# Performance work log

Measured on AMD Instinct MI355X. Metric: run time of the kernel, lower is better.

The kernel has to match this reference:

```python
import jax, jax.numpy as jnp
import numpy as np

N_NODES = 100000
N_EDGES = 640000
DIM = 128
N_LAYERS = 3

def setup_inputs() -> dict:
    key = jax.random.key(0)
    k1, k2, k3 = jax.random.split(key, 3)
    x = jax.random.normal(k1, (1, N_NODES, DIM), dtype=jnp.float32)
    edge_index = jax.random.randint(k2, (2, N_EDGES), 0, N_NODES, dtype=jnp.int64)
    Ws = jax.random.normal(k3, (N_LAYERS, DIM, DIM), dtype=jnp.float32) * (1.0 / np.sqrt(DIM))
    bs = jnp.zeros((N_LAYERS, DIM), dtype=jnp.float32)
    return {"x": x, "edge_index": edge_index, "Ws": Ws, "bs": bs}

def reference(x, edge_index, Ws, bs):
    # Stacked PyG-style GCNConv layers with ReLU, as in GraphEncoder (gnn_type='gcn').
    # GCNConv: add self-loops, symmetric norm D^-1/2 A D^-1/2, h W, scatter-sum, + bias.
    h = x[0]                                  # [N, D] (squeeze batch dim of 1)
    N = h.shape[0]
    loops = jnp.arange(N, dtype=edge_index.dtype)
    src = jnp.concatenate([edge_index[0], loops])   # [E+N] message sources
    dst = jnp.concatenate([edge_index[1], loops])   # [E+N] aggregation targets
    deg = jax.ops.segment_sum(jnp.ones_like(dst, dtype=h.dtype), dst, num_segments=N)
    dinv = jnp.where(deg > 0, jax.lax.rsqrt(deg), 0.0)
    norm = (dinv[src] * dinv[dst])[:, None]         # [E+N, 1] edge weights
    for l in range(Ws.shape[0]):
        m = norm * (h @ Ws[l])[src]                 # gather + per-edge message
        h = jax.ops.segment_sum(m, dst, num_segments=N) + bs[l]
        h = jax.nn.relu(h)
    return h[None]                                  # [1, N, D]
```

## Files before the change

### kernel.cpp

```cpp
#include <hip/hip_runtime.h>

#define DIM 128
#define MROW 272

typedef unsigned int uint32;
typedef short bf16x8 __attribute__((ext_vector_type(8)));
typedef float f32x4 __attribute__((ext_vector_type(4)));

__device__ __forceinline__ unsigned short f2b(float f) {
    return (unsigned short)((__float_as_uint(f) + 0x8000u) >> 16);
}
__device__ __forceinline__ uint32 packbf2(float lo, float hi) {
    uint32 a = __float_as_uint(lo);
    uint32 b = __float_as_uint(hi);
    return ((a + 0x8000u) >> 16) | ((b + 0x8000u) & 0xffff0000u);
}
__device__ __forceinline__ float bflo(uint32 u) { return __uint_as_float(u << 16); }
__device__ __forceinline__ float bfhi(uint32 u) { return __uint_as_float(u & 0xffff0000u); }

__global__ __launch_bounds__(256) void k_count(const int* __restrict__ dst,
                                               int* __restrict__ cnt, int E) {
    int e = blockIdx.x * 256 + threadIdx.x;
    if (e < E) atomicAdd(&cnt[dst[e]], 1);
}

__global__ __launch_bounds__(256) void k_scaleg(const float* __restrict__ x,
                                                const float* __restrict__ dinv,
                                                uint32* __restrict__ g, int n) {
    int t = blockIdx.x * 256 + threadIdx.x;
    if (t >= n * 64) return;
    int node = t >> 6;
    float dv = dinv[node];
    float2 v = ((const float2*)x)[t];
    g[t] = packbf2(dv * v.x, dv * v.y);
}

__global__ __launch_bounds__(256) void k_scan1(const int* __restrict__ cnt,
                                               int* __restrict__ incl,
                                               int* __restrict__ bsums,
                                               float* __restrict__ dinv, int n) {
    __shared__ int tmp[256];
    int i = blockIdx.x * 256 + threadIdx.x;
    int t = threadIdx.x;
    int c = (i < n) ? cnt[i] : 0;
    if (i < n) dinv[i] = rsqrtf((float)(c + 1));
    tmp[t] = c;
    __syncthreads();
#pragma unroll
    for (int off = 1; off < 256; off <<= 1) {
        int v = (t >= off) ? tmp[t - off] : 0;
        __syncthreads();
        tmp[t] += v;
        __syncthreads();
    }
    if (i < n) incl[i] = tmp[t];
    if (t == 255) bsums[blockIdx.x] = tmp[255];
}

__global__ __launch_bounds__(512) void k_scan2(int* __restrict__ bsums, int nb) {
    __shared__ int tmp[512];
    int t = threadIdx.x;
    tmp[t] = (t < nb) ? bsums[t] : 0;
    __syncthreads();
#pragma unroll
    for (int off = 1; off < 512; off <<= 1) {
        int v = (t >= off) ? tmp[t - off] : 0;
        __syncthreads();
        tmp[t] += v;
        __syncthreads();
    }
    if (t < nb) bsums[t] = (t == 0) ? 0 : tmp[t - 1];
}

__global__ __launch_bounds__(256) void k_scan3(int* __restrict__ incl,
                                               const int* __restrict__ bsums, int n) {
    int i = blockIdx.x * 256 + threadIdx.x;
    if (i < n) incl[i] += bsums[blockIdx.x];
}

__global__ __launch_bounds__(256) void k_fill(const int* __restrict__ src,
                                              const int* __restrict__ dst,
                                              int* __restrict__ incl,
                                              int* __restrict__ srcs, int E) {
    int e = blockIdx.x * 256 + threadIdx.x;
    if (e >= E) return;
    int p = atomicSub(&incl[dst[e]], 1) - 1;
    srcs[p] = src[e];
}

__global__ __launch_bounds__(256) void k_prepW(const float* __restrict__ Ws,
                                               short* __restrict__ Wb, int total) {
    int t = blockIdx.x * 256 + threadIdx.x;
    if (t >= total) return;
    int layer = t >> 14;
    int idx = t & 16383;
    int j = idx & 7;
    int l = (idx >> 3) & 63;
    int f = idx >> 9;
    int ks = f & 3;
    int cs = (f >> 2) & 1;
    int w = f >> 3;
    int nn = w * 32 + cs * 16 + (l & 15);
    int kk = ks * 32 + (l >> 4) * 8 + j;
    Wb[t] = (short)f2b(Ws[(size_t)layer * DIM * DIM + kk * DIM + nn]);
}

__global__ __launch_bounds__(256) void k_layer(const uint32* __restrict__ g,
                                               const int* __restrict__ srcs,
                                               const int* __restrict__ rowptr,
                                               const float* __restrict__ dinv,
                                               const short* __restrict__ Wb,
                                               const float* __restrict__ bias,
                                               uint32* __restrict__ Gn,
                                               float* __restrict__ Out,
                                               int n, int E, int final_layer) {
    __shared__ __align__(16) char smem[32 * MROW];
    int tid = threadIdx.x;
    int row0 = blockIdx.x * 32;
    int w = tid >> 6;
    int l = tid & 63;
    int lr = l & 15;
    int lg = l >> 4;

    const bf16x8* wb = (const bf16x8*)Wb;
    bf16x8 bfrag[2][4];
#pragma unroll
    for (int cs = 0; cs < 2; ++cs)
#pragma unroll
        for (int ks = 0; ks < 4; ++ks)
            bfrag[cs][ks] = wb[((w * 2 + cs) * 4 + ks) * 64 + l];

    int hw = tid >> 5;
    int sub = tid & 31;
    const uint2* g2 = (const uint2*)g;
#pragma unroll
    for (int i = 0; i < 4; ++i) {
        int nl = hw * 4 + i;
        int node = row0 + nl;
        uint2 o = make_uint2(0u, 0u);
        if (node < n) {
            int start = rowptr[node];
            int end = (node + 1 < n) ? rowptr[node + 1] : E;
            uint2 us = g2[(size_t)node * 32 + sub];
            float a0 = bflo(us.x), a1 = bfhi(us.x), a2 = bflo(us.y), a3 = bfhi(us.y);
            int p = start;
            for (; p + 4 <= end; p += 4) {
                int s0 = srcs[p + 0];
                int s1 = srcs[p + 1];
                int s2 = srcs[p + 2];
                int s3 = srcs[p + 3];
                uint2 u0 = g2[(size_t)s0 * 32 + sub];
                uint2 u1 = g2[(size_t)s1 * 32 + sub];
                uint2 u2 = g2[(size_t)s2 * 32 + sub];
                uint2 u3 = g2[(size_t)s3 * 32 + sub];
                a0 += bflo(u0.x) + bflo(u1.x) + bflo(u2.x) + bflo(u3.x);
                a1 += bfhi(u0.x) + bfhi(u1.x) + bfhi(u2.x) + bfhi(u3.x);
                a2 += bflo(u0.y) + bflo(u1.y) + bflo(u2.y) + bflo(u3.y);
                a3 += bfhi(u0.y) + bfhi(u1.y) + bfhi(u2.y) + bfhi(u3.y);
            }
            for (; p < end; ++p) {
                uint2 u = g2[(size_t)srcs[p] * 32 + sub];
                a0 += bflo(u.x);
                a1 += bfhi(u.x);
                a2 += bflo(u.y);
                a3 += bfhi(u.y);
            }
            float di = dinv[node];
            o.x = packbf2(di * a0, di * a1);
            o.y = packbf2(di * a2, di * a3);
        }
        *(uint2*)(smem + nl * MROW + sub * 8) = o;
    }
    __syncthreads();

    f32x4 acc[2][2];
#pragma unroll
    for (int rs = 0; rs < 2; ++rs)
#pragma unroll
        for (int cs = 0; cs < 2; ++cs) acc[rs][cs] = (f32x4){0.f, 0.f, 0.f, 0.f};

    const char* base0 = smem + lr * MROW + lg * 16;
    const char* base1 = smem + (16 + lr) * MROW + lg * 16;
#pragma unroll
    for (int ks = 0; ks < 4; ++ks) {
        bf16x8 a0 = *(const bf16x8*)(base0 + ks * 64);
        bf16x8 a1 = *(const bf16x8*)(base1 + ks * 64);
#pragma unroll
        for (int cs = 0; cs < 2; ++cs) {
            acc[0][cs] = __builtin_amdgcn_mfma_f32_16x16x32_bf16(a0, bfrag[cs][ks], acc[0][cs], 0, 0, 0);
            acc[1][cs] = __builtin_amdgcn_mfma_f32_16x16x32_bf16(a1, bfrag[cs][ks], acc[1][cs], 0, 0, 0);
        }
    }

    float b0 = bias[w * 32 + lr];
    float b1 = bias[w * 32 + 16 + lr];

#pragma unroll
    for (int rs = 0; rs < 2; ++rs)
#pragma unroll
        for (int r = 0; r < 4; ++r) {
            int grow = row0 + rs * 16 + lg * 4 + r;
            if (grow < n) {
                float h0 = fmaxf(acc[rs][0][r] + b0, 0.f);
                float h1 = fmaxf(acc[rs][1][r] + b1, 0.f);
                if (final_layer) {
                    Out[(size_t)grow * DIM + w * 32 + lr]      = h0;
                    Out[(size_t)grow * DIM + w * 32 + 16 + lr] = h1;
                } else {
                    float dv = dinv[grow];
                    unsigned short* gp = (unsigned short*)Gn;
                    gp[(size_t)grow * DIM + w * 32 + lr]      = f2b(dv * h0);
                    gp[(size_t)grow * DIM + w * 32 + 16 + lr] = f2b(dv * h1);
                }
            }
        }
}

extern "C" void kernel_launch(void* const* d_in, const int* in_sizes, int n_in,
                              void* d_out, int out_size, void* d_ws, size_t ws_size,
                              hipStream_t stream) {
    const float* x  = (const float*)d_in[0];
    const int*   ei = (const int*)d_in[1];
    const float* Ws = (const float*)d_in[2];
    const float* bs = (const float*)d_in[3];

    const int N = in_sizes[0] / DIM;
    const int E = in_sizes[1] / 2;
    const int L = in_sizes[2] / (DIM * DIM);

    const int* src = ei;
    const int* dst = ei + E;

    float* out = (float*)d_out;

    char* ws = (char*)d_ws;
    uint32* g0   = (uint32*)ws;                ws += (size_t)N * 64 * 4;
    uint32* g1   = (uint32*)ws;                ws += (size_t)N * 64 * 4;
    short* Wb    = (short*)ws;                 ws += (size_t)L * 16384 * 2;
    float* dinv  = (float*)ws;                 ws += (size_t)N * 4;
    int*   cnt   = (int*)ws;                   ws += (size_t)N * 4;
    int*   incl  = (int*)ws;                   ws += (size_t)N * 4;
    int*   srcs  = (int*)ws;                   ws += (size_t)E * 4;
    int*   bsums = (int*)ws;                   ws += 512 * 4;

    const int nbN = (N + 255) / 256;
    const int nbE = (E + 255) / 256;
    const int totW = L * 16384;

    k_prepW<<<(totW + 255) / 256, 256, 0, stream>>>(Ws, Wb, totW);
    hipMemsetAsync(cnt, 0, (size_t)N * 4, stream);
    k_count<<<nbE, 256, 0, stream>>>(dst, cnt, E);
    k_scan1<<<nbN, 256, 0, stream>>>(cnt, incl, bsums, dinv, N);
    k_scan2<<<1, 512, 0, stream>>>(bsums, nbN);
    k_scaleg<<<(N * 64 + 255) / 256, 256, 0, stream>>>(x, dinv, g0, N);
    k_scan3<<<nbN, 256, 0, stream>>>(incl, bsums, N);
    k_fill <<<nbE, 256, 0, stream>>>(src, dst, incl, srcs, E);

    const int nblk = (N + 31) / 32;
    uint32* gin = g0;
    for (int l = 0; l < L; ++l) {
        uint32* gout = (gin == g0) ? g1 : g0;
        k_layer<<<nblk, 256, 0, stream>>>(gin, srcs, incl, dinv,
                                          Wb + (size_t)l * 16384,
                                          bs + (size_t)l * DIM,
                                          gout, out, N, E, l == L - 1);
        gin = gout;
    }
}
```

Measured before the change: 340.7 us.

## Balance edge aggregation across waves with merge-path split and LDS atomics

Replaces the fixed four-nodes-per-half-wave gather with an edge-balanced split: each wave takes an equal slice of the block's CSR edge range, accumulates runs per destination row, and flushes partial sums into an fp32 LDS tile with atomics. Self-loop rows are preloaded into the tile, and dinv scaling plus bf16 conversion move into the MFMA A-fragment load. The aim is to remove load imbalance from skewed degrees. In exchange, each lane now gathers 4 bytes instead of 8, LDS atomics are added, and the tile is twice as large in fp32.

```diff
diff --git a/kernel.cpp b/kernel.cpp
--- a/kernel.cpp
+++ b/kernel.cpp
@@ -1,7 +1,7 @@
 #include <hip/hip_runtime.h>
 
 #define DIM 128
-#define MROW 272
+#define TSTR 132
 
 typedef unsigned int uint32;
 typedef short bf16x8 __attribute__((ext_vector_type(8)));
@@ -114,13 +114,12 @@
                                                uint32* __restrict__ Gn,
                                                float* __restrict__ Out,
                                                int n, int E, int final_layer) {
-    __shared__ __align__(16) char smem[32 * MROW];
+    __shared__ __align__(16) float tile[32 * TSTR];
+    __shared__ int rowS[33];
     int tid = threadIdx.x;
+    int w = tid >> 6;
+    int lane = tid & 63;
     int row0 = blockIdx.x * 32;
-    int w = tid >> 6;
-    int l = tid & 63;
-    int lr = l & 15;
-    int lg = l >> 4;
 
     const bf16x8* wb = (const bf16x8*)Wb;
     bf16x8 bfrag[2][4];
@@ -128,63 +127,96 @@
     for (int cs = 0; cs < 2; ++cs)
 #pragma unroll
         for (int ks = 0; ks < 4; ++ks)
-            bfrag[cs][ks] = wb[((w * 2 + cs) * 4 + ks) * 64 + l];
-
-    int hw = tid >> 5;
-    int sub = tid & 31;
-    const uint2* g2 = (const uint2*)g;
-#pragma unroll
-    for (int i = 0; i < 4; ++i) {
-        int nl = hw * 4 + i;
-        int node = row0 + nl;
-        uint2 o = make_uint2(0u, 0u);
-        if (node < n) {
-            int start = rowptr[node];
-            int end = (node + 1 < n) ? rowptr[node + 1] : E;
-            uint2 us = g2[(size_t)node * 32 + sub];
-            float a0 = bflo(us.x), a1 = bfhi(us.x), a2 = bflo(us.y), a3 = bfhi(us.y);
-            int p = start;
-            for (; p + 4 <= end; p += 4) {
+            bfrag[cs][ks] = wb[((w * 2 + cs) * 4 + ks) * 64 + lane];
+
+    if (tid < 33) {
+        int r = row0 + tid;
+        rowS[tid] = (r < n) ? rowptr[r] : E;
+    }
+#pragma unroll
+    for (int i = 0; i < 8; ++i) {
+        int rl = w * 8 + i;
+        int node = row0 + rl;
+        uint32 u = (node < n) ? g[(size_t)node * 64 + lane] : 0u;
+        *(float2*)(tile + rl * TSTR + 2 * lane) = make_float2(bflo(u), bfhi(u));
+    }
+    __syncthreads();
+
+    {
+        int rs = rowS[0], re = rowS[32];
+        int sz = (re - rs + 3) >> 2;
+        int p0 = rs + w * sz;
+        int p1 = min(p0 + sz, re);
+        if (p0 < p1) {
+            int j = 0;
+            while (rowS[j + 1] <= p0) ++j;
+            int bnd = rowS[j + 1];
+            float a0 = 0.f, a1 = 0.f;
+            int p = p0;
+
+#define STEP(T, VV)                                                    \
+            {                                                          \
+                if (p + (T) >= bnd) {                                  \
+                    atomicAdd(&tile[j * TSTR + 2 * lane], a0);         \
+                    atomicAdd(&tile[j * TSTR + 2 * lane + 1], a1);     \
+                    a0 = 0.f; a1 = 0.f;                                \
+                    do { ++j; bnd = rowS[j + 1]; } while (p + (T) >= bnd); \
+                }                                                      \
+                a0 += bflo(VV); a1 += bfhi(VV);                        \
+            }
+
+            for (; p + 4 <= p1; p += 4) {
                 int s0 = srcs[p + 0];
                 int s1 = srcs[p + 1];
                 int s2 = srcs[p + 2];
                 int s3 = srcs[p + 3];
-                uint2 u0 = g2[(size_t)s0 * 32 + sub];
-                uint2 u1 = g2[(size_t)s1 * 32 + sub];
-                uint2 u2 = g2[(size_t)s2 * 32 + sub];
-                uint2 u3 = g2[(size_t)s3 * 32 + sub];
-                a0 += bflo(u0.x) + bflo(u1.x) + bflo(u2.x) + bflo(u3.x);
-                a1 += bfhi(u0.x) + bfhi(u1.x) + bfhi(u2.x) + bfhi(u3.x);
-                a2 += bflo(u0.y) + bflo(u1.y) + bflo(u2.y) + bflo(u3.y);
-                a3 += bfhi(u0.y) + bfhi(u1.y) + bfhi(u2.y) + bfhi(u3.y);
+                uint32 v0 = g[(size_t)s0 * 64 + lane];
+                uint32 v1 = g[(size_t)s1 * 64 + lane];
+                uint32 v2 = g[(size_t)s2 * 64 + lane];
+                uint32 v3 = g[(size_t)s3 * 64 + lane];
+                STEP(0, v0) STEP(1, v1) STEP(2, v2) STEP(3, v3)
             }
-            for (; p < end; ++p) {
-                uint2 u = g2[(size_t)srcs[p] * 32 + sub];
-                a0 += bflo(u.x);
-                a1 += bfhi(u.x);
-                a2 += bflo(u.y);
-                a3 += bfhi(u.y);
+            for (; p < p1; ++p) {
+                uint32 v = g[(size_t)srcs[p] * 64 + lane];
+                STEP(0, v)
             }
-            float di = dinv[node];
-            o.x = packbf2(di * a0, di * a1);
-            o.y = packbf2(di * a2, di * a3);
+#undef STEP
+            atomicAdd(&tile[j * TSTR + 2 * lane], a0);
+            atomicAdd(&tile[j * TSTR + 2 * lane + 1], a1);
         }
-        *(uint2*)(smem + nl * MROW + sub * 8) = o;
     }
     __syncthreads();
 
+    int lr = lane & 15;
+    int lg = lane >> 4;
+    int n0 = row0 + lr;
+    int n1 = row0 + 16 + lr;
+    float dA = (n0 < n) ? dinv[n0] : 0.f;
+    float dB = (n1 < n) ? dinv[n1] : 0.f;
+
     f32x4 acc[2][2];
 #pragma unroll
     for (int rs = 0; rs < 2; ++rs)
 #pragma unroll
         for (int cs = 0; cs < 2; ++cs) acc[rs][cs] = (f32x4){0.f, 0.f, 0.f, 0.f};
 
-    const char* base0 = smem + lr * MROW + lg * 16;
-    const char* base1 = smem + (16 + lr) * MROW + lg * 16;
 #pragma unroll
     for (int ks = 0; ks < 4; ++ks) {
-        bf16x8 a0 = *(const bf16x8*)(base0 + ks * 64);
-        bf16x8 a1 = *(const bf16x8*)(base1 + ks * 64);
+        const float* t0 = tile + lr * TSTR + ks * 32 + lg * 8;
+        const float* t1 = tile + (16 + lr) * TSTR + ks * 32 + lg * 8;
+        float4 xa = *(const float4*)t0;
+        float4 xb = *(const float4*)(t0 + 4);
+        float4 ya = *(const float4*)t1;
+        float4 yb = *(const float4*)(t1 + 4);
+        bf16x8 a0, a1;
+        a0[0] = (short)f2b(dA * xa.x); a0[1] = (short)f2b(dA * xa.y);
+        a0[2] = (short)f2b(dA * xa.z); a0[3] = (short)f2b(dA * xa.w);
+        a0[4] = (short)f2b(dA * xb.x); a0[5] = (short)f2b(dA * xb.y);
+        a0[6] = (short)f2b(dA * xb.z); a0[7] = (short)f2b(dA * xb.w);
+        a1[0] = (short)f2b(dB * ya.x); a1[1] = (short)f2b(dB * ya.y);
+        a1[2] = (short)f2b(dB * ya.z); a1[3] = (short)f2b(dB * ya.w);
+        a1[4] = (short)f2b(dB * yb.x); a1[5] = (short)f2b(dB * yb.y);
+        a1[6] = (short)f2b(dB * yb.z); a1[7] = (short)f2b(dB * yb.w);
 #pragma unroll
         for (int cs = 0; cs < 2; ++cs) {
             acc[0][cs] = __builtin_amdgcn_mfma_f32_16x16x32_bf16(a0, bfrag[cs][ks], acc[0][cs], 0, 0, 0);
```

New measurement: 462.9 us. 35.9% more time.
